# Kernel optimization log

Hardware: AMD Instinct MI355X
Metric: run time of the kernel (lower is better)

The kernel has to match this reference:

```python
import jax, jax.numpy as jnp
import numpy as np

EPS = 1e-08

def setup_inputs() -> dict:
    key = jax.random.key(0)
    k1, k2 = jax.random.split(key)
    h = jax.random.normal(k1, (4, 4096, 2048), dtype=jnp.float32)
    vectors = jax.random.normal(k2, (16, 2048), dtype=jnp.float32) * 0.01
    return {"h": h, "vectors": vectors}

def reference(h, vectors):
    # Chain of k Householder reflections applied sequentially (loop-carried h).
    def step(h, v):
        v_norm_sq = jnp.maximum(jnp.dot(v, v), EPS)
        proj = jnp.einsum('bsd,d->bs', h, v)  # [B,S]
        h = h - (2.0 / v_norm_sq) * proj[..., None] * v
        return h, None
    h, _ = jax.lax.scan(step, h, vectors)
    return h
```

## Files before the change

### kernel.cpp

```cpp
#include <hip/hip_runtime.h>

#define HH_EPS 1e-8f

constexpr int D     = 2048;
constexpr int K     = 16;
constexpr int RR    = 4;
constexpr int CH    = D / (64 * 4);
constexpr int NROWS = 4 * 4096;
constexpr int WPB   = 4;
constexpr int SPAD  = 17;

__global__ void __launch_bounds__(64) hh_gram_kernel(const float* __restrict__ vecs,
                                                     float* __restrict__ G) {
    int i = blockIdx.x >> 4, j = blockIdx.x & 15;
    int lane = threadIdx.x;
    const float4* a = (const float4*)(vecs + i * D);
    const float4* b = (const float4*)(vecs + j * D);
    float s = 0.f;
#pragma unroll
    for (int c = 0; c < CH; ++c) {
        float4 x = a[c * 64 + lane], y = b[c * 64 + lane];
        s += x.x * y.x + x.y * y.y + x.z * y.z + x.w * y.w;
    }
#pragma unroll
    for (int off = 32; off >= 1; off >>= 1) s += __shfl_xor(s, off);
    if (lane == 0) G[i * K + j] = s;
}

__global__ void __launch_bounds__(256) hh_buildT_kernel(const float* __restrict__ G,
                                                        float* __restrict__ T) {
    __shared__ float sG[K * K], sT[K * K];
    int t = threadIdx.x;
    sG[t] = G[t]; sT[t] = 0.f;
    __syncthreads();
    for (int k = 0; k < K; ++k) {
        float beta = 2.f / fmaxf(sG[k * K + k], HH_EPS);
        if (t == k) sT[k * K + k] = beta;
        else if (t < k) {
            float s = 0.f;
            for (int j = t; j < k; ++j) s += sT[t * K + j] * sG[j * K + k];
            sT[t * K + k] = -beta * s;
        }
        __syncthreads();
    }
    T[t] = sT[t];
}

__device__ __forceinline__ void wy_dot_phase(const float4 (&h)[RR][CH],
                                             const float4 (&vc)[CH], float4 (&vn)[CH],
                                             const float4* __restrict__ v4,
                                             int knext, int lane,
                                             float* __restrict__ myP, int k) {
#pragma unroll
    for (int j = 0; j < CH; ++j)
        vn[j] = v4[knext * (D / 4) + j * 64 + lane];
#pragma unroll
    for (int r = 0; r < RR; ++r) {
        float ax = 0.f, ay = 0.f, az = 0.f, aw = 0.f;
#pragma unroll
        for (int j = 0; j < CH; ++j) {
            ax += h[r][j].x * vc[j].x; ay += h[r][j].y * vc[j].y;
            az += h[r][j].z * vc[j].z; aw += h[r][j].w * vc[j].w;
        }
        float s = (ax + ay) + (az + aw);
        s += __shfl_xor(s, 32);
        s += __shfl_xor(s, 16);
        if (lane < 16) myP[(r * K + k) * SPAD + lane] = s;
    }
}

__device__ __forceinline__ void wy_upd_phase(float4 (&h)[RR][CH],
                                             const float4 (&vc)[CH], float4 (&vn)[CH],
                                             const float4* __restrict__ v4,
                                             int knext, int lane,
                                             const float* __restrict__ myW, int k) {
#pragma unroll
    for (int j = 0; j < CH; ++j)
        vn[j] = v4[knext * (D / 4) + j * 64 + lane];
#pragma unroll
    for (int r = 0; r < RR; ++r) {
        const float w = myW[r * K + k];
#pragma unroll
        for (int j = 0; j < CH; ++j) {
            h[r][j].x -= w * vc[j].x; h[r][j].y -= w * vc[j].y;
            h[r][j].z -= w * vc[j].z; h[r][j].w -= w * vc[j].w;
        }
    }
}

__global__ void __launch_bounds__(256, 2)
hh_apply_wy(const float* __restrict__ h_in, const float* __restrict__ vecs,
            const float* __restrict__ Tmat, float* __restrict__ h_out) {
    __shared__ float sP[WPB * RR * K * SPAD];
    __shared__ float sD[WPB * RR * K];
    __shared__ float sW[WPB * RR * K];
    __shared__ float sT[K * K];

    const int t    = threadIdx.x;
    const int wv   = t >> 6;
    const int lane = t & 63;
    const int gw   = blockIdx.x * WPB + wv;
    const size_t rbase = (size_t)gw * RR;

    float4 h[RR][CH];
    const float4* hin4 = (const float4*)h_in;
#pragma unroll
    for (int r = 0; r < RR; ++r)
#pragma unroll
        for (int j = 0; j < CH; ++j)
            h[r][j] = hin4[(rbase + r) * (D / 4) + j * 64 + lane];

    const float4* v4 = (const float4*)vecs;
    float4 va[CH], vb[CH];
#pragma unroll
    for (int j = 0; j < CH; ++j) va[j] = v4[j * 64 + lane];

    sT[t] = Tmat[t];
    __syncthreads();

    float* myP = sP + wv * (RR * K * SPAD);
    float* myD = sD + wv * (RR * K);
    float* myW = sW + wv * (RR * K);

#pragma unroll 1
    for (int k = 0; k < K; k += 2) {
        wy_dot_phase(h, va, vb, v4, (k + 1) & 15, lane, myP, k);
        wy_dot_phase(h, vb, va, v4, (k + 2) & 15, lane, myP, k + 1);
    }

    const int kk  = lane & 15;
    const int seg = lane >> 4;
#pragma unroll
    for (int r = 0; r < RR; ++r) {
        float s = 0.f;
#pragma unroll
        for (int i = 0; i < 4; ++i)
            s += myP[(r * K + kk) * SPAD + seg * 4 + i];
        s += __shfl_xor(s, 16);
        s += __shfl_xor(s, 32);
        if (lane < 16) myD[r * K + kk] = s;
    }

#pragma unroll
    for (int r = 0; r < RR; ++r) {
        float wsum = 0.f;
#pragma unroll
        for (int k2 = 0; k2 < K; ++k2)
            wsum += myD[r * K + k2] * sT[k2 * K + kk];
        if (lane < 16) myW[r * K + kk] = wsum;
    }

#pragma unroll 1
    for (int k = 0; k < K; k += 2) {
        wy_upd_phase(h, va, vb, v4, (k + 1) & 15, lane, myW, k);
        wy_upd_phase(h, vb, va, v4, (k + 2) & 15, lane, myW, k + 1);
    }

#pragma unroll
    for (int r = 0; r < RR; ++r) {
        float4* row = (float4*)h_out + (rbase + r) * (D / 4);
#pragma unroll
        for (int j = 0; j < CH; ++j)
            row[j * 64 + lane] = h[r][j];
    }
}

extern "C" void kernel_launch(void* const* d_in, const int* in_sizes, int n_in,
                              void* d_out, int out_size, void* d_ws, size_t ws_size,
                              hipStream_t stream) {
    const float* h    = (const float*)d_in[0];
    const float* vecs = (const float*)d_in[1];
    float* out        = (float*)d_out;

    float* G  = (float*)d_ws;
    float* Tm = G + K * K;

    hh_gram_kernel<<<K * K, 64, 0, stream>>>(vecs, G);
    hh_buildT_kernel<<<1, 256, 0, stream>>>(G, Tm);

    int blocks = NROWS / (RR * WPB);
    hh_apply_wy<<<blocks, 256, 0, stream>>>(h, vecs, Tm, out);
}
```

Before: 266.3 us.

## Halve rows per wave, drop double-buffered vectors to raise occupancy

Each wave now holds 2 rows of h in registers instead of 4. The two vector buffers are merged into one, refilled element by element as each chunk is consumed. Launch bounds rise from 2 to 4 blocks per CU to cut register pressure and gain occupancy for latency hiding. The cost is that each loaded Householder vector is reused across fewer rows, so vector loads per row go up, and the in-place reload gives less lead time to hide load latency.

```diff
diff --git a/kernel.cpp b/kernel.cpp
--- a/kernel.cpp
+++ b/kernel.cpp
@@ -4,7 +4,7 @@
 
 constexpr int D     = 2048;
 constexpr int K     = 16;
-constexpr int RR    = 4;
+constexpr int RR    = 2;
 constexpr int CH    = D / (64 * 4);
 constexpr int NROWS = 4 * 4096;
 constexpr int WPB   = 4;
@@ -47,48 +47,48 @@
 }
 
 __device__ __forceinline__ void wy_dot_phase(const float4 (&h)[RR][CH],
-                                             const float4 (&vc)[CH], float4 (&vn)[CH],
+                                             float4 (&va)[CH],
                                              const float4* __restrict__ v4,
                                              int knext, int lane,
                                              float* __restrict__ myP, int k) {
+    float a0x = 0.f, a0y = 0.f, a0z = 0.f, a0w = 0.f;
+    float a1x = 0.f, a1y = 0.f, a1z = 0.f, a1w = 0.f;
 #pragma unroll
-    for (int j = 0; j < CH; ++j)
-        vn[j] = v4[knext * (D / 4) + j * 64 + lane];
-#pragma unroll
-    for (int r = 0; r < RR; ++r) {
-        float ax = 0.f, ay = 0.f, az = 0.f, aw = 0.f;
-#pragma unroll
-        for (int j = 0; j < CH; ++j) {
-            ax += h[r][j].x * vc[j].x; ay += h[r][j].y * vc[j].y;
-            az += h[r][j].z * vc[j].z; aw += h[r][j].w * vc[j].w;
-        }
-        float s = (ax + ay) + (az + aw);
-        s += __shfl_xor(s, 32);
-        s += __shfl_xor(s, 16);
-        if (lane < 16) myP[(r * K + k) * SPAD + lane] = s;
+    for (int j = 0; j < CH; ++j) {
+        float4 v = va[j];
+        a0x += h[0][j].x * v.x; a0y += h[0][j].y * v.y;
+        a0z += h[0][j].z * v.z; a0w += h[0][j].w * v.w;
+        a1x += h[1][j].x * v.x; a1y += h[1][j].y * v.y;
+        a1z += h[1][j].z * v.z; a1w += h[1][j].w * v.w;
+        va[j] = v4[knext * (D / 4) + j * 64 + lane];
+    }
+    float s0 = (a0x + a0y) + (a0z + a0w);
+    float s1 = (a1x + a1y) + (a1z + a1w);
+    s0 += __shfl_xor(s0, 32); s0 += __shfl_xor(s0, 16);
+    s1 += __shfl_xor(s1, 32); s1 += __shfl_xor(s1, 16);
+    if (lane < 16) {
+        myP[(0 * K + k) * SPAD + lane] = s0;
+        myP[(1 * K + k) * SPAD + lane] = s1;
     }
 }
 
 __device__ __forceinline__ void wy_upd_phase(float4 (&h)[RR][CH],
-                                             const float4 (&vc)[CH], float4 (&vn)[CH],
+                                             float4 (&va)[CH],
                                              const float4* __restrict__ v4,
                                              int knext, int lane,
-                                             const float* __restrict__ myW, int k) {
+                                             float w0, float w1) {
 #pragma unroll
-    for (int j = 0; j < CH; ++j)
-        vn[j] = v4[knext * (D / 4) + j * 64 + lane];
-#pragma unroll
-    for (int r = 0; r < RR; ++r) {
-        const float w = myW[r * K + k];
-#pragma unroll
-        for (int j = 0; j < CH; ++j) {
-            h[r][j].x -= w * vc[j].x; h[r][j].y -= w * vc[j].y;
-            h[r][j].z -= w * vc[j].z; h[r][j].w -= w * vc[j].w;
-        }
+    for (int j = 0; j < CH; ++j) {
+        float4 v = va[j];
+        h[0][j].x -= w0 * v.x; h[0][j].y -= w0 * v.y;
+        h[0][j].z -= w0 * v.z; h[0][j].w -= w0 * v.w;
+        h[1][j].x -= w1 * v.x; h[1][j].y -= w1 * v.y;
+        h[1][j].z -= w1 * v.z; h[1][j].w -= w1 * v.w;
+        va[j] = v4[knext * (D / 4) + j * 64 + lane];
     }
 }
 
-__global__ void __launch_bounds__(256, 2)
+__global__ void __launch_bounds__(256, 4)
 hh_apply_wy(const float* __restrict__ h_in, const float* __restrict__ vecs,
             const float* __restrict__ Tmat, float* __restrict__ h_out) {
     __shared__ float sP[WPB * RR * K * SPAD];
@@ -111,7 +111,7 @@
             h[r][j] = hin4[(rbase + r) * (D / 4) + j * 64 + lane];
 
     const float4* v4 = (const float4*)vecs;
-    float4 va[CH], vb[CH];
+    float4 va[CH];
 #pragma unroll
     for (int j = 0; j < CH; ++j) va[j] = v4[j * 64 + lane];
 
@@ -123,10 +123,8 @@
     float* myW = sW + wv * (RR * K);
 
 #pragma unroll 1
-    for (int k = 0; k < K; k += 2) {
-        wy_dot_phase(h, va, vb, v4, (k + 1) & 15, lane, myP, k);
-        wy_dot_phase(h, vb, va, v4, (k + 2) & 15, lane, myP, k + 1);
-    }
+    for (int k = 0; k < K; ++k)
+        wy_dot_phase(h, va, v4, (k + 1) & 15, lane, myP, k);
 
     const int kk  = lane & 15;
     const int seg = lane >> 4;
@@ -151,9 +149,10 @@
     }
 
 #pragma unroll 1
-    for (int k = 0; k < K; k += 2) {
-        wy_upd_phase(h, va, vb, v4, (k + 1) & 15, lane, myW, k);
-        wy_upd_phase(h, vb, va, v4, (k + 2) & 15, lane, myW, k + 1);
+    for (int k = 0; k < K; ++k) {
+        float w0 = myW[0 * K + k];
+        float w1 = myW[1 * K + k];
+        wy_upd_phase(h, va, v4, (k + 1) & 15, lane, w0, w1);
     }
 
 #pragma unroll
```

Result: slower. 297.8 us (+11.8%).
